# Optimization experiments

Hardware: AMD Instinct MI355X
Metric: run time of the kernel (lower is better)

## Reference

```python
import jax, jax.numpy as jnp
import numpy as np


def setup_inputs() -> dict:
    key = jax.random.key(0)
    k1, k2, k3 = jax.random.split(key, 3)
    B, Cin, H, Wd = 8, 32, 96, 96
    Cout = 32
    v = jax.random.normal(k1, (B, Cin, H, Wd), dtype=jnp.float32)
    W = jax.random.normal(k2, (Cout, Cin), dtype=jnp.float32) / np.sqrt(Cin)
    b = jax.random.normal(k3, (Cout,), dtype=jnp.float32) * 0.01
    return {"v": v, "W": W, "b": b}


def reference(v, W, b):
    B, Cin, y_res, x_res = v.shape
    Cout = W.shape[0]
    N = y_res * x_res
    # meshgrid with indexing='xy': shapes (y_res, x_res)
    xs = jnp.linspace(0.0, 1.0, x_res, dtype=v.dtype)
    ys = jnp.linspace(0.0, 1.0, y_res, dtype=v.dtype)
    x_coords, y_coords = jnp.meshgrid(xs, ys)  # (y_res, x_res)
    coords = jnp.stack((x_coords, y_coords), axis=0)  # (2, y, x)
    # pairwise diffs: (2, y, x, y, x)
    diff = coords[:, None, None, :, :] - coords[:, :, :, None, None]
    dist = jnp.sqrt(jnp.sum(diff * diff, axis=0))  # (y, x, y, x)
    dist = dist.reshape(y_res, x_res, N)  # (y, x, N)
    # linear projection on channel-last features
    vp = jnp.transpose(v, (0, 2, 3, 1))  # (B, y, x, Cin)
    t = (vp @ W.T + b).reshape(B, N, Cout)  # (B, N, Cout)
    # integral operator: contract over all N discretization points
    up = jnp.einsum('bdo,yxd->byxo', t, dist)  # (B, y, x, Cout)
    u = jnp.transpose(up, (0, 3, 1, 2))  # (B, Cout, y, x)
    return u
```

## Files before the change

kernel.cpp:

```cpp
#include <hip/hip_runtime.h>
#include <hip/hip_bf16.h>


typedef __bf16    bf16x8 __attribute__((ext_vector_type(8)));
typedef float     f32x4  __attribute__((ext_vector_type(4)));
typedef float     f32x16 __attribute__((ext_vector_type(16)));
typedef _Float16  f16x4  __attribute__((ext_vector_type(4)));
typedef _Float16  f16x8  __attribute__((ext_vector_type(8)));

#define NPTS   9216
#define CIN    32
#define COUT   32
#define NCOLS  256
#define SCALE  (1.0f / 95.0f)
#define OUTN   (NCOLS * NPTS)
#define NSPLIT 7
#define KCHUNK 1344

__global__ __launch_bounds__(256) void proj_kernel(
    const float* __restrict__ v, const float* __restrict__ W,
    const float* __restrict__ bias, __bf16* __restrict__ T2)
{
    __shared__ float Wl[COUT * CIN];
    __shared__ float bl[COUT];
    const int t = threadIdx.x;
    for (int i = t; i < COUT * CIN; i += 256) Wl[i] = W[i];
    if (t < COUT) bl[t] = bias[t];
    __syncthreads();

    const int b = blockIdx.y;
    const int d = blockIdx.x * 256 + t;
    const float* vb = v + (size_t)b * CIN * NPTS + d;

    float acc[COUT];
#pragma unroll
    for (int o = 0; o < COUT; ++o) acc[o] = bl[o];
#pragma unroll 4
    for (int c = 0; c < CIN; ++c) {
        const float vv = vb[(size_t)c * NPTS];
#pragma unroll
        for (int o = 0; o < COUT; ++o) acc[o] += vv * Wl[o * CIN + c];
    }
#pragma unroll
    for (int o = 0; o < COUT; ++o)
        T2[(size_t)(b * COUT + o) * NPTS + d] = (__bf16)acc[o];
}

__device__ __forceinline__ bf16x8 agen(float dx, float dy2) {
    float f[8];
#pragma unroll
    for (int j = 0; j < 8; ++j) {
        f[j] = __builtin_amdgcn_sqrtf(__builtin_fmaf(dx, dx, dy2));
        dx -= SCALE;
    }
    union { unsigned int u[4]; bf16x8 v; } pk;
#pragma unroll
    for (int q = 0; q < 4; ++q) {
        const unsigned int lo = __builtin_bit_cast(unsigned int, f[2*q])   + 0x8000u;
        const unsigned int hi = __builtin_bit_cast(unsigned int, f[2*q+1]) + 0x8000u;
        pk.u[q] = __builtin_amdgcn_perm(hi, lo, 0x07060302u);
    }
    return pk.v;
}

__global__ __launch_bounds__(256, 4) void gemm_kernel(
    const __bf16* __restrict__ T2, void* __restrict__ dst, int usePartial)
{
    __shared__ __align__(1024) unsigned char lds[2][16384];

    const int tid  = threadIdx.x;
    const int wid  = tid >> 6;
    const int lane = tid & 63;
    const int l31  = lane & 31;
    const int hi   = lane >> 5;

    const int bid = blockIdx.x;
    const int z   = bid % NSPLIT;
    const int rem = bid / NSPLIT;
    const int cb  = rem & 1;
    const int x   = rem >> 1;
    const int koff = z * KCHUNK;
    const int nt   = (z == NSPLIT - 1) ? 18 : 21;
    const int colBase = cb * 128;

    const int prow = x * 128 + wid * 32 + l31;
    const int yp = prow / 96, xp = prow - yp * 96;
    const int xph = xp - hi * 8;

    int boff[4][4];
#pragma unroll
    for (int s = 0; s < 4; ++s)
#pragma unroll
        for (int n = 0; n < 4; ++n) {
            const int col  = n * 32 + l31;
            const int slot = (s * 2 + hi) ^ (col & 7);
            boff[s][n] = col * 128 + slot * 16;
        }

    const int scol = tid >> 3;
    const int sch  = (tid & 7) ^ (scol & 7);
    const __bf16* gsrc = T2 + (size_t)(colBase + scol) * NPTS + koff + sch * 8;
    const int ldst = tid * 16;

    auto stage = [&](unsigned char* buf, int kt) {
#pragma unroll
        for (int i = 0; i < 4; ++i)
            __builtin_amdgcn_global_load_lds(
                (const __attribute__((address_space(1))) void*)
                    (gsrc + (size_t)kt * 64 + (size_t)i * 32 * NPTS),
                (__attribute__((address_space(3))) void*)
                    (buf + i * 4096 + ldst),
                16, 0, 0);
    };

    f32x16 acc[4];
#pragma unroll
    for (int n = 0; n < 4; ++n) acc[n] = (f32x16)(0.0f);

    stage(lds[0], 0);
    __syncthreads();

    int xt = 0, yt = z * 14;
    int cur = 0;
    for (int kt = 0; kt < nt; ++kt) {
        if (kt + 1 < nt) stage(lds[cur ^ 1], kt + 1);
        const unsigned char* Lb = lds[cur];

#pragma unroll
        for (int s = 0; s < 4; ++s) {
            const int xr = xt + s * 16;
            const int xk = (xr >= 96) ? xr - 96 : xr;
            const int yk = (xr >= 96) ? yt + 1  : yt;
            const float dy = (float)(yp - yk) * SCALE;
            const bf16x8 a = agen((float)(xph - xk) * SCALE, dy * dy);
#pragma unroll
            for (int n = 0; n < 4; ++n) {
                const bf16x8 b = *(const bf16x8*)(Lb + boff[s][n]);
                acc[n] = __builtin_amdgcn_mfma_f32_32x32x16_bf16(
                    a, b, acc[n], 0, 0, 0);
            }
        }
        xt += 64; if (xt >= 96) { xt -= 96; ++yt; }
        __syncthreads();
        cur ^= 1;
    }

    const int rowb = x * 128 + wid * 32;
    if (usePartial) {
        _Float16* pb = (_Float16*)dst + (size_t)z * OUTN;
#pragma unroll
        for (int n = 0; n < 4; ++n) {
            const int col = colBase + n * 32 + l31;
            _Float16* ob = pb + (size_t)col * NPTS + rowb + 4 * hi;
#pragma unroll
            for (int q = 0; q < 4; ++q) {
                f16x4 h = { (_Float16)acc[n][4*q],
                            (_Float16)acc[n][4*q+1],
                            (_Float16)acc[n][4*q+2],
                            (_Float16)acc[n][4*q+3] };
                *(f16x4*)(ob + q * 8) = h;
            }
        }
    } else {
        float* ob0 = (float*)dst;
#pragma unroll
        for (int n = 0; n < 4; ++n) {
            const int col = colBase + n * 32 + l31;
            float* ob = ob0 + (size_t)col * NPTS + rowb + 4 * hi;
#pragma unroll
            for (int q = 0; q < 4; ++q)
#pragma unroll
                for (int r = 0; r < 4; ++r)
                    atomicAdd(ob + q * 8 + r, acc[n][4*q+r]);
        }
    }
}

__global__ __launch_bounds__(256) void reduce_kernel(
    const _Float16* __restrict__ part, float* __restrict__ out)
{
    const size_t i = ((size_t)blockIdx.x * 256 + threadIdx.x) * 8;
    float a[8] = {};
#pragma unroll
    for (int s = 0; s < NSPLIT; ++s) {
        f16x8 v = *(const f16x8*)(part + (size_t)s * OUTN + i);
#pragma unroll
        for (int r = 0; r < 8; ++r) a[r] += (float)v[r];
    }
    f32x4 o0 = { a[0], a[1], a[2], a[3] };
    f32x4 o1 = { a[4], a[5], a[6], a[7] };
    *(f32x4*)(out + i)     = o0;
    *(f32x4*)(out + i + 4) = o1;
}

extern "C" void kernel_launch(void* const* d_in, const int* in_sizes, int n_in,
                              void* d_out, int out_size, void* d_ws, size_t ws_size,
                              hipStream_t stream) {
    const float* v    = (const float*)d_in[0];
    const float* W    = (const float*)d_in[1];
    const float* bias = (const float*)d_in[2];
    float* out = (float*)d_out;

    __bf16* T2 = (__bf16*)d_ws;
    const size_t t2b = (size_t)NCOLS * NPTS * 2;
    _Float16* partial = (_Float16*)((char*)d_ws + t2b);
    const size_t need = t2b + (size_t)NSPLIT * OUTN * 2;
    const int usePartial = (ws_size >= need) ? 1 : 0;

    proj_kernel<<<dim3(36, 8), 256, 0, stream>>>(v, W, bias, T2);
    if (usePartial) {
        gemm_kernel<<<72 * 2 * NSPLIT, 256, 0, stream>>>(T2, partial, 1);
        reduce_kernel<<<OUTN / 2048, 256, 0, stream>>>(partial, out);
    } else {
        hipMemsetAsync(d_out, 0, (size_t)out_size * sizeof(float), stream);
        gemm_kernel<<<72 * 2 * NSPLIT, 256, 0, stream>>>(T2, out, 0);
    }
}
```

Baseline: 83.32 us.

## Widen gemm block tile to all 256 columns to reuse generated distance fragments

Each gemm block now computes all 256 output columns instead of 128, so the on-the-fly sqrt distance A-fragment is computed once per k-step and reused across eight MFMA column tiles. Grid size halves, LDS staging buffers double and the accumulator register count doubles, with launch bounds lowered to 2 blocks per CU. This trades lower occupancy and fewer blocks for halving redundant distance generation and duplicate A work.

```diff
diff --git a/kernel.cpp b/kernel.cpp
--- a/kernel.cpp
+++ b/kernel.cpp
@@ -63,10 +63,10 @@
     return pk.v;
 }
 
-__global__ __launch_bounds__(256, 4) void gemm_kernel(
+__global__ __launch_bounds__(256, 2) void gemm_kernel(
     const __bf16* __restrict__ T2, void* __restrict__ dst, int usePartial)
 {
-    __shared__ __align__(1024) unsigned char lds[2][16384];
+    __shared__ __align__(1024) unsigned char lds[2][32768];
 
     const int tid  = threadIdx.x;
     const int wid  = tid >> 6;
@@ -75,23 +75,21 @@
     const int hi   = lane >> 5;
 
     const int bid = blockIdx.x;
-    const int z   = bid % NSPLIT;
-    const int rem = bid / NSPLIT;
-    const int cb  = rem & 1;
-    const int x   = rem >> 1;
+    const int z   = bid / 72;
+    const int x   = bid - z * 72;
     const int koff = z * KCHUNK;
     const int nt   = (z == NSPLIT - 1) ? 18 : 21;
-    const int colBase = cb * 128;
-
-    const int prow = x * 128 + wid * 32 + l31;
+
+    const int pbase = x * 128 + wid * 32;
+    const int prow  = pbase + l31;
     const int yp = prow / 96, xp = prow - yp * 96;
     const int xph = xp - hi * 8;
 
-    int boff[4][4];
+    int boff[4][8];
 #pragma unroll
     for (int s = 0; s < 4; ++s)
 #pragma unroll
-        for (int n = 0; n < 4; ++n) {
+        for (int n = 0; n < 8; ++n) {
             const int col  = n * 32 + l31;
             const int slot = (s * 2 + hi) ^ (col & 7);
             boff[s][n] = col * 128 + slot * 16;
@@ -99,31 +97,31 @@
 
     const int scol = tid >> 3;
     const int sch  = (tid & 7) ^ (scol & 7);
-    const __bf16* gsrc = T2 + (size_t)(colBase + scol) * NPTS + koff + sch * 8;
+    const __bf16* gsrc = T2 + (size_t)scol * NPTS + koff + sch * 8;
     const int ldst = tid * 16;
 
-    auto stage = [&](unsigned char* buf, int kt) {
-#pragma unroll
-        for (int i = 0; i < 4; ++i)
+    auto stage = [&](int buf, int kt) {
+#pragma unroll
+        for (int i = 0; i < 8; ++i)
             __builtin_amdgcn_global_load_lds(
                 (const __attribute__((address_space(1))) void*)
                     (gsrc + (size_t)kt * 64 + (size_t)i * 32 * NPTS),
                 (__attribute__((address_space(3))) void*)
-                    (buf + i * 4096 + ldst),
+                    (&lds[buf][i * 4096 + ldst]),
                 16, 0, 0);
     };
 
-    f32x16 acc[4];
-#pragma unroll
-    for (int n = 0; n < 4; ++n) acc[n] = (f32x16)(0.0f);
-
-    stage(lds[0], 0);
+    f32x16 acc[8];
+#pragma unroll
+    for (int n = 0; n < 8; ++n) acc[n] = (f32x16)(0.0f);
+
+    stage(0, 0);
     __syncthreads();
 
     int xt = 0, yt = z * 14;
     int cur = 0;
     for (int kt = 0; kt < nt; ++kt) {
-        if (kt + 1 < nt) stage(lds[cur ^ 1], kt + 1);
+        if (kt + 1 < nt) stage(cur ^ 1, kt + 1);
         const unsigned char* Lb = lds[cur];
 
 #pragma unroll
@@ -134,7 +132,7 @@
             const float dy = (float)(yp - yk) * SCALE;
             const bf16x8 a = agen((float)(xph - xk) * SCALE, dy * dy);
 #pragma unroll
-            for (int n = 0; n < 4; ++n) {
+            for (int n = 0; n < 8; ++n) {
                 const bf16x8 b = *(const bf16x8*)(Lb + boff[s][n]);
                 acc[n] = __builtin_amdgcn_mfma_f32_32x32x16_bf16(
                     a, b, acc[n], 0, 0, 0);
@@ -145,13 +143,12 @@
         cur ^= 1;
     }
 
-    const int rowb = x * 128 + wid * 32;
     if (usePartial) {
         _Float16* pb = (_Float16*)dst + (size_t)z * OUTN;
 #pragma unroll
-        for (int n = 0; n < 4; ++n) {
-            const int col = colBase + n * 32 + l31;
-            _Float16* ob = pb + (size_t)col * NPTS + rowb + 4 * hi;
+        for (int n = 0; n < 8; ++n) {
+            const int col = n * 32 + l31;
+            _Float16* ob = pb + (size_t)col * NPTS + pbase + 4 * hi;
 #pragma unroll
             for (int q = 0; q < 4; ++q) {
                 f16x4 h = { (_Float16)acc[n][4*q],
@@ -164,9 +161,9 @@
     } else {
         float* ob0 = (float*)dst;
 #pragma unroll
-        for (int n = 0; n < 4; ++n) {
-            const int col = colBase + n * 32 + l31;
-            float* ob = ob0 + (size_t)col * NPTS + rowb + 4 * hi;
+        for (int n = 0; n < 8; ++n) {
+            const int col = n * 32 + l31;
+            float* ob = ob0 + (size_t)col * NPTS + pbase + 4 * hi;
 #pragma unroll
             for (int q = 0; q < 4; ++q)
 #pragma unroll
@@ -209,10 +206,10 @@
 
     proj_kernel<<<dim3(36, 8), 256, 0, stream>>>(v, W, bias, T2);
     if (usePartial) {
-        gemm_kernel<<<72 * 2 * NSPLIT, 256, 0, stream>>>(T2, partial, 1);
+        gemm_kernel<<<72 * NSPLIT, 256, 0, stream>>>(T2, partial, 1);
         reduce_kernel<<<OUTN / 2048, 256, 0, stream>>>(partial, out);
     } else {
         hipMemsetAsync(d_out, 0, (size_t)out_size * sizeof(float), stream);
-        gemm_kernel<<<72 * 2 * NSPLIT, 256, 0, stream>>>(T2, out, 0);
-    }
-}
+        gemm_kernel<<<72 * NSPLIT, 256, 0, stream>>>(T2, out, 0);
+    }
+}
```

New measurement: 78.63 us, median of 2. 5.6% less time.
